# Performance work log

Hardware: AMD Instinct MI355X
Metric: run time of the kernel (lower is better)

Reference implementation:

```python
import jax, jax.numpy as jnp
import numpy as np

N_NODES = 100000
N_EDGES = 1600000
IN_FEATS = 256
H_FEATS = 128
N_CLASSES = 40


def setup_inputs() -> dict:
    key = jax.random.key(0)
    ks = jax.random.split(key, 6)
    in_feat = jax.random.normal(ks[0], (N_NODES, IN_FEATS), dtype=jnp.float32)
    src = jax.random.randint(ks[1], (N_EDGES,), 0, N_NODES, dtype=jnp.int32)
    dst = jax.random.randint(ks[2], (N_EDGES,), 0, N_NODES, dtype=jnp.int32)
    # Glorot-ish init for the two GraphConv weights
    W1 = jax.random.normal(ks[3], (IN_FEATS, H_FEATS), dtype=jnp.float32) * (1.0 / np.sqrt(IN_FEATS))
    b1 = jnp.zeros((H_FEATS,), dtype=jnp.float32)
    W2 = jax.random.normal(ks[4], (H_FEATS, N_CLASSES), dtype=jnp.float32) * (1.0 / np.sqrt(H_FEATS))
    b2 = jnp.zeros((N_CLASSES,), dtype=jnp.float32)
    return {"in_feat": in_feat, "src": src, "dst": dst,
            "W1": W1, "b1": b1, "W2": W2, "b2": b2}


def _degree_isqrt(idx, n):
    # degree per node, clamped to >=1 (DGL norm='both' behavior), then ^-1/2
    deg = jax.ops.segment_sum(jnp.ones_like(idx, dtype=jnp.float32), idx, num_segments=n)
    return jax.lax.rsqrt(jnp.maximum(deg, 1.0))


def _graph_conv(x, W, b, src, dst, out_isqrt, in_isqrt, n):
    # DGL GraphConv norm='both', weight applied before aggregation
    h = (x @ W) * out_isqrt[:, None]            # [N, F_out]
    m = jax.ops.segment_sum(h[src], dst, num_segments=n)  # gather+scatter over edges
    return m * in_isqrt[:, None] + b


def reference(in_feat, src, dst, W1, b1, W2, b2):
    n = in_feat.shape[0]
    out_isqrt = _degree_isqrt(src, n)  # out-degree norm for source nodes
    in_isqrt = _degree_isqrt(dst, n)   # in-degree norm for destination nodes
    h = _graph_conv(in_feat, W1, b1, src, dst, out_isqrt, in_isqrt, n)
    h = jax.nn.relu(h)
    h = _graph_conv(h, W2, b2, src, dst, out_isqrt, in_isqrt, n)
    return h
```

## Files before the change

### kernel.cpp

```cpp
#include <hip/hip_runtime.h>
#include <hip/hip_bf16.h>
#include <stdint.h>

#define NN 100000
#define NE 1600000
#define INF 256
#define HF 128
#define NC 40
#define NNP 100352
#define NBUK 784
#define BKSH 7
#define NBLK 128
#define CHUNK 12500

typedef unsigned short ushort_t;
typedef unsigned int uint_t;
typedef unsigned char uchar_t;
typedef __attribute__((ext_vector_type(8))) short short8;
typedef __attribute__((ext_vector_type(4))) float f32x4;

__device__ __forceinline__ float bflo(uint_t u) {
    union { uint_t i; float f; } v; v.i = u << 16; return v.f;
}
__device__ __forceinline__ float bfhi(uint_t u) {
    union { uint_t i; float f; } v; v.i = u & 0xffff0000u; return v.f;
}
__device__ __forceinline__ uint_t f2bf(float f) {
    __hip_bfloat16 h = __float2bfloat16(f);
    return (uint_t)*reinterpret_cast<ushort_t*>(&h);
}

__launch_bounds__(256)
__global__ void k_bcount(const int* __restrict__ src, const int* __restrict__ dst,
                         uint_t* __restrict__ countsA, uint_t* __restrict__ countsB,
                         const float* __restrict__ W1, ushort_t* __restrict__ W1f,
                         const float* __restrict__ W2, ushort_t* __restrict__ W2f) {
    __shared__ uint_t hA[NBUK], hB[NBUK];
    for (int t = threadIdx.x; t < NBUK; t += 256) { hA[t] = 0; hB[t] = 0; }

    int i = blockIdx.x * 256 + threadIdx.x;
    {
        int k = i >> 7, n = i & 127;
        int ks = k >> 5, q = (k >> 3) & 3, j = k & 7;
        int ct = n >> 4, ln = n & 15;
        W1f[(((ks * 8 + ct) * 4 + q) * 16 + ln) * 8 + j] = (ushort_t)f2bf(W1[i]);
    }
    if (i < HF * 48) {
        int k = i / 48, n = i % 48;
        int ks = k >> 5, q = (k >> 3) & 3, j = k & 7;
        int ct = n >> 4, ln = n & 15;
        float v = (n < NC) ? W2[k * NC + n] : 0.0f;
        W2f[(((ks * 3 + ct) * 4 + q) * 16 + ln) * 8 + j] = (ushort_t)f2bf(v);
    }
    __syncthreads();

    const int beg = blockIdx.x * CHUNK, end = beg + CHUNK;
    for (int e = beg + threadIdx.x; e < end; e += 256) {
        atomicAdd(&hA[(uint_t)dst[e] >> BKSH], 1u);
        atomicAdd(&hB[(uint_t)src[e] >> BKSH], 1u);
    }
    __syncthreads();
    for (int t = threadIdx.x; t < NBUK; t += 256) {
        if (hA[t]) atomicAdd(&countsA[t], hA[t]);
        if (hB[t]) atomicAdd(&countsB[t], hB[t]);
    }
}

__global__ void k_bscan(const uint_t* __restrict__ countsA, const uint_t* __restrict__ countsB,
                        uint_t* __restrict__ basesA, uint_t* __restrict__ basesB,
                        uint_t* __restrict__ cursA, uint_t* __restrict__ cursB) {
    __shared__ uint_t s[1024];
    const int t = threadIdx.x;
    uint_t v = (t < NBUK) ? countsA[t] : 0;
    s[t] = v; __syncthreads();
    for (int off = 1; off < 1024; off <<= 1) {
        uint_t tv = (t >= off) ? s[t - off] : 0;
        __syncthreads();
        s[t] += tv;
        __syncthreads();
    }
    if (t < NBUK) { uint_t e = s[t] - v; basesA[t] = e; cursA[t] = e; }
    if (t == 0) basesA[NBUK] = NE;
    __syncthreads();
    v = (t < NBUK) ? countsB[t] : 0;
    s[t] = v; __syncthreads();
    for (int off = 1; off < 1024; off <<= 1) {
        uint_t tv = (t >= off) ? s[t - off] : 0;
        __syncthreads();
        s[t] += tv;
        __syncthreads();
    }
    if (t < NBUK) { uint_t e = s[t] - v; basesB[t] = e; cursB[t] = e; }
    if (t == 0) basesB[NBUK] = NE;
}

__launch_bounds__(256)
__global__ void k_bfill(const int* __restrict__ src, const int* __restrict__ dst,
                        uint_t* __restrict__ cursA, uint_t* __restrict__ cursB,
                        uint_t* __restrict__ edgesA, uchar_t* __restrict__ bytesB) {
    __shared__ uint_t hA[NBUK], hB[NBUK];
    for (int t = threadIdx.x; t < NBUK; t += 256) { hA[t] = 0; hB[t] = 0; }
    __syncthreads();
    const int beg = blockIdx.x * CHUNK, end = beg + CHUNK;
    for (int e = beg + threadIdx.x; e < end; e += 256) {
        atomicAdd(&hA[(uint_t)dst[e] >> BKSH], 1u);
        atomicAdd(&hB[(uint_t)src[e] >> BKSH], 1u);
    }
    __syncthreads();
    for (int t = threadIdx.x; t < NBUK; t += 256) {
        uint_t c = hA[t];
        hA[t] = c ? atomicAdd(&cursA[t], c) : 0;
        c = hB[t];
        hB[t] = c ? atomicAdd(&cursB[t], c) : 0;
    }
    __syncthreads();
    for (int e = beg + threadIdx.x; e < end; e += 256) {
        uint_t d = (uint_t)dst[e], s = (uint_t)src[e];
        uint_t pA = atomicAdd(&hA[d >> BKSH], 1u);
        edgesA[pA] = ((d & 127u) << 17) | s;
        uint_t pB = atomicAdd(&hB[s >> BKSH], 1u);
        bytesB[pB] = (uchar_t)(s & 127u);
    }
}

__launch_bounds__(256)
__global__ void k_bfinish(const uint_t* __restrict__ basesA, const uint_t* __restrict__ basesB,
                          const uint_t* __restrict__ edgesA, const uchar_t* __restrict__ bytesB,
                          int* __restrict__ row_ptr, int* __restrict__ srcs,
                          float* __restrict__ isq_d, float* __restrict__ isq_s) {
    __shared__ uint_t h[128], sc[128], cur[128];
    const int b = blockIdx.x, t = threadIdx.x;
    const uint_t beg = basesA[b], end = basesA[b + 1];
    if (t < 128) h[t] = 0;
    __syncthreads();
    for (uint_t e = beg + t; e < end; e += 256)
        atomicAdd(&h[(edgesA[e] >> 17) & 127u], 1u);
    __syncthreads();
    uint_t v = (t < 128) ? h[t] : 0;
    if (t < 128) sc[t] = v;
    __syncthreads();
    for (int off = 1; off < 128; off <<= 1) {
        uint_t tv = (t >= off && t < 128) ? sc[t - off] : 0;
        __syncthreads();
        if (t < 128) sc[t] += tv;
        __syncthreads();
    }
    if (t < 128) {
        uint_t excl = sc[t] - v;
        row_ptr[b * 128 + t] = (int)(beg + excl);
        isq_d[b * 128 + t] = rsqrtf(fmaxf((float)v, 1.0f));
        cur[t] = excl;
    }
    __syncthreads();
    for (uint_t e = beg + t; e < end; e += 256) {
        uint_t u = edgesA[e];
        uint_t p = atomicAdd(&cur[(u >> 17) & 127u], 1u);
        srcs[beg + p] = (int)(u & 0x1FFFFu);
    }
    __syncthreads();
    if (t < 128) h[t] = 0;
    __syncthreads();
    const uint_t begB = basesB[b], endB = basesB[b + 1];
    for (uint_t e = begB + t; e < endB; e += 256)
        atomicAdd(&h[bytesB[e]], 1u);
    __syncthreads();
    if (t < 128) isq_s[b * 128 + t] = rsqrtf(fmaxf((float)h[t], 1.0f));
}

__launch_bounds__(256)
__global__ void k_gemm1(const float* __restrict__ X, const ushort_t* __restrict__ W1f,
                        const float* __restrict__ isq_s, ushort_t* __restrict__ H) {
    const int wv = threadIdx.x >> 6;
    const int lane = threadIdx.x & 63;
    const int ln = lane & 15;
    const int q  = lane >> 4;
    const int r0 = blockIdx.x * 64 + wv * 16;
    const int rm = min(r0 + ln, NN - 1);

    f32x4 acc[8];
#pragma unroll
    for (int ct = 0; ct < 8; ++ct) acc[ct] = (f32x4){0.f, 0.f, 0.f, 0.f};

    const float* xp = &X[(size_t)rm * INF + q * 8];
    const uint4* wf = (const uint4*)W1f;

    for (int ks = 0; ks < 8; ++ks) {
        float4 xa = *(const float4*)xp;
        float4 xb = *(const float4*)(xp + 4);
        xp += 32;
        short8 af;
        af[0] = (short)f2bf(xa.x); af[1] = (short)f2bf(xa.y);
        af[2] = (short)f2bf(xa.z); af[3] = (short)f2bf(xa.w);
        af[4] = (short)f2bf(xb.x); af[5] = (short)f2bf(xb.y);
        af[6] = (short)f2bf(xb.z); af[7] = (short)f2bf(xb.w);
#pragma unroll
        for (int ct = 0; ct < 8; ++ct) {
            union { uint4 u; short8 s; } bv;
            bv.u = wf[(size_t)(ks * 8 + ct) * 64 + lane];
            acc[ct] = __builtin_amdgcn_mfma_f32_16x16x32_bf16(af, bv.s, acc[ct], 0, 0, 0);
        }
    }

#pragma unroll
    for (int reg = 0; reg < 4; ++reg) {
        int r = r0 + q * 4 + reg;
        if (r < NN) {
            float s = isq_s[r];
#pragma unroll
            for (int ct = 0; ct < 8; ++ct)
                H[(size_t)r * HF + ct * 16 + ln] = (ushort_t)f2bf(acc[ct][reg] * s);
        }
    }
}

#define ACC8(v) { a[0] += bflo((v).x); a[1] += bfhi((v).x); \
                  a[2] += bflo((v).y); a[3] += bfhi((v).y); \
                  a[4] += bflo((v).z); a[5] += bfhi((v).z); \
                  a[6] += bflo((v).w); a[7] += bfhi((v).w); }

__launch_bounds__(256)
__global__ void k_agg1_gemm2(const int* __restrict__ row_ptr, const int* __restrict__ srcs,
                             const uint4* __restrict__ H16, const float* __restrict__ isq_d,
                             const float* __restrict__ isq_s, const float* __restrict__ b1,
                             const ushort_t* __restrict__ W2f, ushort_t* __restrict__ H2b) {
    __shared__ uint4 h1s[16][16];
    const int wv = threadIdx.x >> 6;
    const int lane = threadIdx.x & 63;
    const int grp = lane >> 4;
    const int gl  = lane & 15;
    const int n0 = blockIdx.x * 16;

    const float4 bva = ((const float4*)b1)[gl * 2];
    const float4 bvb = ((const float4*)b1)[gl * 2 + 1];

    for (int ni = 0; ni < 4; ++ni) {
        const int rl = wv * 4 + ni;
        const int n = n0 + rl;
        float a[8];
#pragma unroll
        for (int k = 0; k < 8; ++k) a[k] = 0.0f;

        int beg = row_ptr[n], end = row_ptr[n + 1];
        int j = beg;
        for (; j + 16 <= end; j += 16) {
            int sA = srcs[j + grp];
            int sB = srcs[j + 4 + grp];
            int sC = srcs[j + 8 + grp];
            int sD = srcs[j + 12 + grp];
            uint4 vA = H16[(size_t)sA * 16 + gl];
            uint4 vB = H16[(size_t)sB * 16 + gl];
            uint4 vC = H16[(size_t)sC * 16 + gl];
            uint4 vD = H16[(size_t)sD * 16 + gl];
            ACC8(vA); ACC8(vB); ACC8(vC); ACC8(vD);
        }
        for (; j + 8 <= end; j += 8) {
            int sA = srcs[j + grp];
            int sB = srcs[j + 4 + grp];
            uint4 vA = H16[(size_t)sA * 16 + gl];
            uint4 vB = H16[(size_t)sB * 16 + gl];
            ACC8(vA); ACC8(vB);
        }
        for (; j + 4 <= end; j += 4) {
            uint4 v = H16[(size_t)srcs[j + grp] * 16 + gl];
            ACC8(v);
        }
        int r = end - j;
        if (grp < r) {
            uint4 v = H16[(size_t)srcs[j + grp] * 16 + gl];
            ACC8(v);
        }
#pragma unroll
        for (int k = 0; k < 8; ++k) {
            a[k] += __shfl_xor(a[k], 16);
            a[k] += __shfl_xor(a[k], 32);
        }
        if (lane < 16) {
            float sc = isq_d[n];
            uint_t p0 = f2bf(fmaxf(a[0] * sc + bva.x, 0.0f))
                      | (f2bf(fmaxf(a[1] * sc + bva.y, 0.0f)) << 16);
            uint_t p1 = f2bf(fmaxf(a[2] * sc + bva.z, 0.0f))
                      | (f2bf(fmaxf(a[3] * sc + bva.w, 0.0f)) << 16);
            uint_t p2 = f2bf(fmaxf(a[4] * sc + bvb.x, 0.0f))
                      | (f2bf(fmaxf(a[5] * sc + bvb.y, 0.0f)) << 16);
            uint_t p3 = f2bf(fmaxf(a[6] * sc + bvb.z, 0.0f))
                      | (f2bf(fmaxf(a[7] * sc + bvb.w, 0.0f)) << 16);
            h1s[rl][gl ^ rl] = (uint4){p0, p1, p2, p3};
        }
    }
    __syncthreads();

    if (wv < 3) {
        const int q = grp;
        const int ln = gl;
        f32x4 acc = (f32x4){0.f, 0.f, 0.f, 0.f};
        const uint4* wf = (const uint4*)W2f;
#pragma unroll
        for (int ks = 0; ks < 4; ++ks) {
            union { uint4 u; short8 s; } av, bv;
            av.u = h1s[ln][(ks * 4 + q) ^ ln];
            bv.u = wf[(size_t)(ks * 3 + wv) * 64 + lane];
            acc = __builtin_amdgcn_mfma_f32_16x16x32_bf16(av.s, bv.s, acc, 0, 0, 0);
        }
        int c = wv * 16 + ln;
        if (c < NC) {
#pragma unroll
            for (int reg = 0; reg < 4; ++reg) {
                int rg = n0 + q * 4 + reg;
                H2b[(size_t)rg * NC + c] = (ushort_t)f2bf(acc[reg] * isq_s[rg]);
            }
        }
    }
}

__launch_bounds__(256)
__global__ void k_gather2(const int* __restrict__ row_ptr, const int* __restrict__ srcs,
                          const uint4* __restrict__ H2b4, const float* __restrict__ isq_d,
                          const float* __restrict__ b2, float* __restrict__ out) {
    __shared__ float pt[4][64][9];
    const int wv = threadIdx.x >> 6;
    const int lane = threadIdx.x & 63;
    const int grp = lane / 5;
    const int gl  = lane - grp * 5;
    const int n = blockIdx.x * 4 + wv;

    float a[8];
#pragma unroll
    for (int k = 0; k < 8; ++k) a[k] = 0.0f;

    if (n < NN && grp < 12) {
        int beg = row_ptr[n], end = row_ptr[n + 1];
        int j = beg;
        for (; j + 24 <= end; j += 24) {
            int sA = srcs[j + grp];
            int sB = srcs[j + 12 + grp];
            uint4 vA = H2b4[(size_t)sA * 5 + gl];
            uint4 vB = H2b4[(size_t)sB * 5 + gl];
            ACC8(vA); ACC8(vB);
        }
        if (j + 12 <= end) {
            uint4 v = H2b4[(size_t)srcs[j + grp] * 5 + gl];
            ACC8(v);
            j += 12;
        }
        int r = end - j;
        if (grp < r) {
            uint4 v = H2b4[(size_t)srcs[j + grp] * 5 + gl];
            ACC8(v);
        }
    }
#pragma unroll
    for (int k = 0; k < 8; ++k) pt[wv][lane][k] = a[k];
    __syncthreads();

    if (n < NN && lane < NC) {
        const int g2 = lane >> 3;
        const int i2 = lane & 7;
        float s = 0.0f;
#pragma unroll
        for (int g = 0; g < 12; ++g)
            s += pt[wv][g * 5 + g2][i2];
        out[(size_t)n * NC + lane] = s * isq_d[n] + b2[lane];
    }
}

extern "C" void kernel_launch(void* const* d_in, const int* in_sizes, int n_in,
                              void* d_out, int out_size, void* d_ws, size_t ws_size,
                              hipStream_t stream) {
    const float* X  = (const float*)d_in[0];
    const int* src  = (const int*)d_in[1];
    const int* dst  = (const int*)d_in[2];
    const float* W1 = (const float*)d_in[3];
    const float* b1 = (const float*)d_in[4];
    const float* W2 = (const float*)d_in[5];
    const float* b2 = (const float*)d_in[6];
    float* out = (float*)d_out;

    int* w = (int*)d_ws;
    uint_t* countsA = (uint_t*)w;
    uint_t* countsB = countsA + NBUK;
    uint_t* basesA  = countsB + NBUK;
    uint_t* basesB  = basesA + NBUK + 1;
    uint_t* cursA   = basesB + NBUK + 1;
    uint_t* cursB   = cursA + NBUK;
    float* isq_s    = (float*)(w + 8192);
    float* isq_d    = isq_s + NNP;
    int* row_ptr    = (int*)(isq_d + NNP);
    ushort_t* W1f   = (ushort_t*)(row_ptr + NNP);
    ushort_t* W2f   = (ushort_t*)(row_ptr + NNP + 16384);
    int* Hw         = row_ptr + NNP + 16384 + 3072;
    uint_t* edgesA  = (uint_t*)Hw;
    uchar_t* bytesB = (uchar_t*)(Hw + NE);
    ushort_t* H     = (ushort_t*)Hw;
    int* srcs       = Hw + 6400000;
    ushort_t* H2b   = (ushort_t*)(srcs + NE);

    hipMemsetAsync(countsA, 0, 2 * NBUK * sizeof(uint_t), stream);

    k_bcount <<<NBLK, 256, 0, stream>>>(src, dst, countsA, countsB, W1, W1f, W2, W2f);
    k_bscan  <<<1, 1024, 0, stream>>>(countsA, countsB, basesA, basesB, cursA, cursB);
    k_bfill  <<<NBLK, 256, 0, stream>>>(src, dst, cursA, cursB, edgesA, bytesB);
    k_bfinish<<<NBUK, 256, 0, stream>>>(basesA, basesB, edgesA, bytesB,
                                        row_ptr, srcs, isq_d, isq_s);

    k_gemm1<<<(NN + 63) / 64, 256, 0, stream>>>(X, W1f, isq_s, H);

    k_agg1_gemm2<<<NN / 16, 256, 0, stream>>>(row_ptr, srcs, (const uint4*)H,
                                              isq_d, isq_s, b1, W2f, H2b);

    k_gather2<<<(NN + 3) / 4, 256, 0, stream>>>(row_ptr, srcs, (const uint4*)H2b,
                                                isq_d, b2, out);
}
```

Measured before the change: 392.7 us.

## Double counting blocks and prefetch all X rows upfront in GEMM1

Doubles the number of edge-counting blocks and halves each block's edge chunk, adding a guard so the W1 reformat stays within bounds when the grid grows. In the first GEMM, all eight K-slices of X are loaded into registers and converted to bf16 before the MFMA loop, rather than loaded one slice per iteration. This exposes more memory-level parallelism for the X stream. The register-heavy prefetch could reduce occupancy, which the added launch bound of 4 tries to keep in check.

```diff
diff --git a/kernel.cpp b/kernel.cpp
--- a/kernel.cpp
+++ b/kernel.cpp
@@ -10,8 +10,8 @@
 #define NNP 100352
 #define NBUK 784
 #define BKSH 7
-#define NBLK 128
-#define CHUNK 12500
+#define NBLK 256
+#define CHUNK 6250
 
 typedef unsigned short ushort_t;
 typedef unsigned int uint_t;
@@ -39,7 +39,7 @@
     for (int t = threadIdx.x; t < NBUK; t += 256) { hA[t] = 0; hB[t] = 0; }
 
     int i = blockIdx.x * 256 + threadIdx.x;
-    {
+    if (i < INF * HF) {
         int k = i >> 7, n = i & 127;
         int ks = k >> 5, q = (k >> 3) & 3, j = k & 7;
         int ct = n >> 4, ln = n & 15;
@@ -167,7 +167,7 @@
     if (t < 128) isq_s[b * 128 + t] = rsqrtf(fmaxf((float)h[t], 1.0f));
 }
 
-__launch_bounds__(256)
+__launch_bounds__(256, 4)
 __global__ void k_gemm1(const float* __restrict__ X, const ushort_t* __restrict__ W1f,
                         const float* __restrict__ isq_s, ushort_t* __restrict__ H) {
     const int wv = threadIdx.x >> 6;
@@ -184,20 +184,32 @@
     const float* xp = &X[(size_t)rm * INF + q * 8];
     const uint4* wf = (const uint4*)W1f;
 
+    float4 xv[16];
+#pragma unroll
+    for (int t = 0; t < 8; ++t) {
+        xv[2 * t]     = *(const float4*)(xp + t * 32);
+        xv[2 * t + 1] = *(const float4*)(xp + t * 32 + 4);
+    }
+    short8 af[8];
+#pragma unroll
+    for (int t = 0; t < 8; ++t) {
+        af[t][0] = (short)f2bf(xv[2 * t].x);
+        af[t][1] = (short)f2bf(xv[2 * t].y);
+        af[t][2] = (short)f2bf(xv[2 * t].z);
+        af[t][3] = (short)f2bf(xv[2 * t].w);
+        af[t][4] = (short)f2bf(xv[2 * t + 1].x);
+        af[t][5] = (short)f2bf(xv[2 * t + 1].y);
+        af[t][6] = (short)f2bf(xv[2 * t + 1].z);
+        af[t][7] = (short)f2bf(xv[2 * t + 1].w);
+    }
+
+#pragma unroll
     for (int ks = 0; ks < 8; ++ks) {
-        float4 xa = *(const float4*)xp;
-        float4 xb = *(const float4*)(xp + 4);
-        xp += 32;
-        short8 af;
-        af[0] = (short)f2bf(xa.x); af[1] = (short)f2bf(xa.y);
-        af[2] = (short)f2bf(xa.z); af[3] = (short)f2bf(xa.w);
-        af[4] = (short)f2bf(xb.x); af[5] = (short)f2bf(xb.y);
-        af[6] = (short)f2bf(xb.z); af[7] = (short)f2bf(xb.w);
 #pragma unroll
         for (int ct = 0; ct < 8; ++ct) {
             union { uint4 u; short8 s; } bv;
             bv.u = wf[(size_t)(ks * 8 + ct) * 64 + lane];
-            acc[ct] = __builtin_amdgcn_mfma_f32_16x16x32_bf16(af, bv.s, acc[ct], 0, 0, 0);
+            acc[ct] = __builtin_amdgcn_mfma_f32_16x16x32_bf16(af[ks], bv.s, acc[ct], 0, 0, 0);
         }
     }
 
```

Measured after the change: 371.1 us. 5.5% less time.
